# Kernel tuning notes

Measured on AMD Instinct MI355X. Metric: run time of the kernel, lower is better.

## Reference

```python
import jax, jax.numpy as jnp
import numpy as np

N_HEADS = 16


def setup_inputs() -> dict:
    key = jax.random.key(0)
    ks = jax.random.split(key, 5)
    B, S, D = 2, 2048, 1024
    H = N_HEADS
    return {
        "queries": jax.random.normal(ks[0], (B, S, D), dtype=jnp.float32),
        "keys": jax.random.normal(ks[1], (B, S, D), dtype=jnp.float32),
        "values": jax.random.normal(ks[2], (B, S, D), dtype=jnp.float32),
        "bias": jax.random.normal(ks[3], (1, H, S, S), dtype=jnp.float32) * 0.02,
        "w_out": jax.random.normal(ks[4], (D, D), dtype=jnp.float32) * (1.0 / np.sqrt(D)),
    }


def _split_heads(x, n_heads):
    B, S, D = x.shape
    return x.reshape(B, S, n_heads, D // n_heads).transpose(0, 2, 1, 3)  # [B,H,S,hd]


def reference(queries, keys, values, bias, w_out):
    H = N_HEADS
    q = _split_heads(queries, H)
    k = _split_heads(keys, H)
    v = _split_heads(values, H)
    hd = k.shape[-1]
    # NOTE: original adds bias to raw logits, THEN scales by 1/sqrt(dk)
    logits = jnp.einsum("bhqd,bhkd->bhqk", q, k) + bias
    weights = jax.nn.softmax(logits * (1.0 / np.sqrt(hd)), axis=-1)
    attn = jnp.einsum("bhqk,bhkd->bhqd", weights, v)  # [B,H,Sq,hd]
    B, _, Sq, _ = attn.shape
    combined = attn.transpose(0, 2, 1, 3).reshape(B, Sq, H * hd)
    return combined @ w_out
```

## Files before the change

### kernel.cpp

```cpp
#include <hip/hip_runtime.h>

typedef float  f32x4  __attribute__((ext_vector_type(4)));
typedef short  bf16x8 __attribute__((ext_vector_type(8)));
typedef short  s16x4  __attribute__((ext_vector_type(4)));
typedef unsigned int u32x4 __attribute__((ext_vector_type(4)));

#define MFMA_BF16 __builtin_amdgcn_mfma_f32_16x16x32_bf16

__device__ __forceinline__ short f2bf(float f) {
  __bf16 h = (__bf16)f;
  return __builtin_bit_cast(short, h);
}

constexpr int S = 2048, D = 1024, H = 16, HD = 64;
constexpr int NT = S / 64;
constexpr int NTH = NT / 2;
constexpr float SCALE = 0.125f;
constexpr float L2E = 1.44269504f;
constexpr float SL = SCALE * L2E;

#define GLDS16(g, l) __builtin_amdgcn_global_load_lds( \
    (const __attribute__((address_space(1))) unsigned*)(g), \
    (__attribute__((address_space(3))) unsigned*)(l), 16, 0, 0)

#define WAITV(n) asm volatile("s_waitcnt vmcnt(" #n ")" ::: "memory")
#define SBAR()   __builtin_amdgcn_s_barrier()

__global__ __launch_bounds__(256)
void kv_prep(const float* __restrict__ Kg, const float* __restrict__ Vg,
             short* __restrict__ KVb) {
  const int tile = blockIdx.x, h = blockIdx.y, b = blockIdx.z;
  const int t = threadIdx.x, lane = t & 63, w = t >> 6;
  const int lg = lane >> 4, lm = lane & 15;
  __shared__ short kt[64 * 68], vt[64 * 68];
  const float* kp = Kg + ((size_t)(b * S + tile * 64)) * D + h * HD;
  const float* vp = Vg + ((size_t)(b * S + tile * 64)) * D + h * HD;
  #pragma unroll
  for (int i = 0; i < 4; ++i) {
    int idx = i * 256 + t, r = idx >> 4, c4 = (idx & 15) * 4;
    float4 k4 = *(const float4*)(kp + (size_t)r * D + c4);
    s16x4 ks; ks[0]=f2bf(k4.x); ks[1]=f2bf(k4.y); ks[2]=f2bf(k4.z); ks[3]=f2bf(k4.w);
    *(s16x4*)&kt[r * 68 + c4] = ks;
    float4 v4 = *(const float4*)(vp + (size_t)r * D + c4);
    s16x4 vs; vs[0]=f2bf(v4.x); vs[1]=f2bf(v4.y); vs[2]=f2bf(v4.z); vs[3]=f2bf(v4.w);
    *(s16x4*)&vt[r * 68 + c4] = vs;
  }
  __syncthreads();
  const size_t obase = ((size_t)((b * H + h) * NT + tile)) * 8192;
  #pragma unroll
  for (int j = 0; j < 2; ++j) {
    int f = w + j * 4, kk = f >> 2, mf = f & 3;
    int row = mf * 16 + lm, col = kk * 32 + lg * 4;
    s16x4 c0 = *(const s16x4*)&kt[row * 68 + col];
    s16x4 c1 = *(const s16x4*)&kt[row * 68 + col + 16];
    bf16x8 a;
    a[0]=c0[0]; a[1]=c0[1]; a[2]=c0[2]; a[3]=c0[3];
    a[4]=c1[0]; a[5]=c1[1]; a[6]=c1[2]; a[7]=c1[3];
    *(bf16x8*)&KVb[obase + (size_t)(f * 64 + lane) * 8] = a;
  }
  #pragma unroll
  for (int j = 0; j < 2; ++j) {
    int fv = w + j * 4, kk = fv >> 2, of = fv & 3;
    int col = of * 16 + lm;
    bf16x8 a;
    #pragma unroll
    for (int half = 0; half < 2; ++half)
      #pragma unroll
      for (int e = 0; e < 4; ++e)
        a[half * 4 + e] = vt[(kk * 32 + lg * 4 + half * 16 + e) * 68 + col];
    *(bf16x8*)&KVb[obase + (size_t)((8 + fv) * 64 + lane) * 8] = a;
  }
}

__global__ __launch_bounds__(512, 4)
void attn_fused(const float* __restrict__ Qg, const float* __restrict__ Bg,
                const short* __restrict__ KVb,
                float* __restrict__ OP, float* __restrict__ ML) {
  __shared__ __attribute__((aligned(16))) short smem[16384];
  const int bid = blockIdx.x;
  const int c = bid & 7, g = bid >> 3;
  const int qb = g & 7, z = g >> 3;
  const int h = (c << 1) | (z & 1);
  const int b = (z >> 1) & 1;
  const int half = z >> 2;
  const int q0 = qb * 256;
  const int t = threadIdx.x, lane = t & 63, w = t >> 6;
  const int lg = lane >> 4, lm = lane & 15;

  bf16x8 qf[2][2];
  #pragma unroll
  for (int fq = 0; fq < 2; ++fq) {
    const float* qp = Qg + ((size_t)(b * S + q0 + w * 32 + fq * 16 + lm)) * D + h * HD;
    #pragma unroll
    for (int kk = 0; kk < 2; ++kk)
      #pragma unroll
      for (int j = 0; j < 8; ++j)
        qf[fq][kk][j] = f2bf(qp[kk * 32 + (j >> 2) * 16 + lg * 4 + (j & 3)]);
  }

  const short* KVt = KVb + ((size_t)((b * H + h) * NT + half * NTH)) * 8192;
  const float* bp = Bg + ((size_t)(h * S + q0 + w * 32 + lm)) * S + half * (NTH * 64) + lg * 4;

  const f32x4 zero4 = {0.f, 0.f, 0.f, 0.f};
  f32x4 o[2][4];
  #pragma unroll
  for (int fq = 0; fq < 2; ++fq)
    #pragma unroll
    for (int i = 0; i < 4; ++i) o[fq][i] = zero4;
  float M[2] = {-__builtin_inff(), -__builtin_inff()};
  float L[2] = {0.f, 0.f};
  f32x4 sacc[2][4];

#define STAGE(tile, buf)                                                \
  {                                                                     \
    const short* kvg_ = KVt + (size_t)(tile) * 8192;                    \
    _Pragma("unroll")                                                   \
    for (int f_ = 0; f_ < 2; ++f_) {                                    \
      int fr_ = w * 2 + f_;                                             \
      GLDS16(kvg_ + (size_t)(fr_ * 64 + lane) * 8, (buf) + fr_ * 512);  \
    }                                                                   \
  }

#define BLOAD(tile)                                                     \
  {                                                                     \
    _Pragma("unroll")                                                   \
    for (int fq_ = 0; fq_ < 2; ++fq_)                                   \
      _Pragma("unroll")                                                 \
      for (int mf_ = 0; mf_ < 4; ++mf_)                                 \
        sacc[fq_][mf_] = *(const f32x4*)(bp + (size_t)fq_ * 16 * S +    \
                                         (size_t)(tile) * 64 + mf_ * 16); \
  }

  STAGE(0, smem);
  BLOAD(0);

  for (int tt = 0; tt < NTH; ++tt) {
    SBAR();
    if (tt < NTH - 1) {
      STAGE(tt + 1, smem + ((tt + 1) & 1) * 8192);
      WAITV(10);
    } else {
      WAITV(8);
    }
    SBAR();
    const short* buf = smem + (tt & 1) * 8192;

    __builtin_amdgcn_s_setprio(1);
    #pragma unroll
    for (int kk = 0; kk < 2; ++kk)
      #pragma unroll
      for (int mf = 0; mf < 4; ++mf) {
        bf16x8 a = *(const bf16x8*)&buf[(kk * 4 + mf) * 512 + lane * 8];
        sacc[0][mf] = MFMA_BF16(a, qf[0][kk], sacc[0][mf], 0, 0, 0);
        sacc[1][mf] = MFMA_BF16(a, qf[1][kk], sacc[1][mf], 0, 0, 0);
      }
    __builtin_amdgcn_s_setprio(0);

    float tmax[2] = {-__builtin_inff(), -__builtin_inff()};
    #pragma unroll
    for (int fq = 0; fq < 2; ++fq)
      #pragma unroll
      for (int mf = 0; mf < 4; ++mf)
        #pragma unroll
        for (int j = 0; j < 4; ++j) {
          float tv = sacc[fq][mf][j] * SL;
          sacc[fq][mf][j] = tv;
          tmax[fq] = fmaxf(tmax[fq], tv);
        }
    #pragma unroll
    for (int fq = 0; fq < 2; ++fq) {
      tmax[fq] = fmaxf(tmax[fq], __shfl_xor(tmax[fq], 16, 64));
      tmax[fq] = fmaxf(tmax[fq], __shfl_xor(tmax[fq], 32, 64));
    }
    const int skip = (tmax[0] <= M[0]) && (tmax[1] <= M[1]);
    if (!__all(skip)) {
      #pragma unroll
      for (int fq = 0; fq < 2; ++fq) {
        float Mn = fmaxf(M[fq], tmax[fq]);
        float alpha = exp2f(M[fq] - Mn);
        #pragma unroll
        for (int of = 0; of < 4; ++of) {
          o[fq][of][0] *= alpha; o[fq][of][1] *= alpha;
          o[fq][of][2] *= alpha; o[fq][of][3] *= alpha;
        }
        L[fq] *= alpha;
        M[fq] = Mn;
      }
    }
    #pragma unroll
    for (int fq = 0; fq < 2; ++fq) {
      float psum = 0.f;
      #pragma unroll
      for (int mf = 0; mf < 4; ++mf)
        #pragma unroll
        for (int j = 0; j < 4; ++j) {
          float e = exp2f(sacc[fq][mf][j] - M[fq]);
          sacc[fq][mf][j] = e;
          psum += e;
        }
      psum += __shfl_xor(psum, 16, 64);
      psum += __shfl_xor(psum, 32, 64);
      L[fq] += psum;
    }
    bf16x8 pb[2][2];
    #pragma unroll
    for (int fq = 0; fq < 2; ++fq)
      #pragma unroll
      for (int kk = 0; kk < 2; ++kk)
        #pragma unroll
        for (int j = 0; j < 8; ++j)
          pb[fq][kk][j] = f2bf(sacc[fq][kk * 2 + (j >> 2)][j & 3]);

    if (tt < NTH - 1) BLOAD(tt + 1);

    __builtin_amdgcn_s_setprio(1);
    #pragma unroll
    for (int kk = 0; kk < 2; ++kk)
      #pragma unroll
      for (int of = 0; of < 4; ++of) {
        bf16x8 a = *(const bf16x8*)&buf[4096 + (kk * 4 + of) * 512 + lane * 8];
        o[0][of] = MFMA_BF16(a, pb[0][kk], o[0][of], 0, 0, 0);
        o[1][of] = MFMA_BF16(a, pb[1][kk], o[1][of], 0, 0, 0);
      }
    __builtin_amdgcn_s_setprio(0);
  }

  const int p = ((b * H + h) << 3) | qb;
  float* opb = OP + ((size_t)(half * 256 + p)) * 16384 + w * 2048;
  #pragma unroll
  for (int fq = 0; fq < 2; ++fq)
    #pragma unroll
    for (int of = 0; of < 4; ++of)
      *(f32x4*)&opb[(fq * 4 + of) * 256 + lane * 4] = o[fq][of];
  float* mlb = ML + ((size_t)(half * 256 + p)) * 512;
  if (lane < 16) {
    mlb[w * 32 + lm]        = M[0];
    mlb[w * 32 + 16 + lm]   = M[1];
    mlb[256 + w * 32 + lm]      = L[0];
    mlb[256 + w * 32 + 16 + lm] = L[1];
  }
#undef STAGE
#undef BLOAD
}

__global__ __launch_bounds__(256)
void combine(const float* __restrict__ OP, const float* __restrict__ ML,
             short* __restrict__ comb) {
  const int w = blockIdx.x & 7, p = blockIdx.x >> 3;
  const int b = p >> 7, h = (p >> 3) & 15, qb = p & 7;
  const int t = threadIdx.x, lane = t & 63, fr2 = t >> 6;
  __shared__ __attribute__((aligned(16))) short tile[32 * 72];
  const float* op0 = OP + (size_t)p * 16384 + w * 2048;
  const float* op1 = OP + (size_t)(256 + p) * 16384 + w * 2048;
  const float* ml0 = ML + (size_t)p * 512;
  const float* ml1 = ML + (size_t)(256 + p) * 512;
  #pragma unroll
  for (int ff = 0; ff < 2; ++ff) {
    int f = fr2 + ff * 4, fq = f >> 2, of = f & 3;
    int ql = fq * 16 + (lane & 15);
    int d  = of * 16 + (lane >> 4) * 4;
    float m0 = ml0[w * 32 + ql], m1 = ml1[w * 32 + ql];
    float l0 = ml0[256 + w * 32 + ql], l1 = ml1[256 + w * 32 + ql];
    float m = fmaxf(m0, m1);
    float a0 = exp2f(m0 - m), a1 = exp2f(m1 - m);
    float inv = 1.f / (l0 * a0 + l1 * a1);
    f32x4 v0 = *(const f32x4*)&op0[f * 256 + lane * 4];
    f32x4 v1 = *(const f32x4*)&op1[f * 256 + lane * 4];
    s16x4 r;
    #pragma unroll
    for (int j = 0; j < 4; ++j)
      r[j] = f2bf((v0[j] * a0 + v1[j] * a1) * inv);
    *(s16x4*)&tile[ql * 72 + d] = r;
  }
  __syncthreads();
  const int row = t >> 3, seg = t & 7;
  u32x4 u = *(const u32x4*)&tile[row * 72 + seg * 8];
  *(u32x4*)&comb[((size_t)(b * S + qb * 256 + w * 32 + row)) * D + h * HD + seg * 8] = u;
}

__global__ __launch_bounds__(256)
void wt_kernel(const float* __restrict__ W, short* __restrict__ Wt) {
  __shared__ __attribute__((aligned(16))) short tile[64 * 72];
  const int n0 = blockIdx.x * 64, k0 = blockIdx.y * 64;
  const int t = threadIdx.x;
  #pragma unroll
  for (int i = 0; i < 4; ++i) {
    int idx = i * 256 + t;
    int r  = idx >> 4, c4 = (idx & 15) * 4;
    float4 wv = *(const float4*)(W + (size_t)(k0 + r) * D + n0 + c4);
    tile[(c4 + 0) * 72 + r] = f2bf(wv.x);
    tile[(c4 + 1) * 72 + r] = f2bf(wv.y);
    tile[(c4 + 2) * 72 + r] = f2bf(wv.z);
    tile[(c4 + 3) * 72 + r] = f2bf(wv.w);
  }
  __syncthreads();
  #pragma unroll
  for (int it = 0; it < 2; ++it) {
    int idx = it * 256 + t;
    int r = idx >> 3, seg = idx & 7;
    u32x4 u = *(const u32x4*)&tile[r * 72 + seg * 8];
    *(u32x4*)&Wt[(size_t)(n0 + r) * D + k0 + seg * 8] = u;
  }
}

__device__ __forceinline__ bf16x8 ld_frag_swz(const short* base, int row, int kk, int lg) {
  const char* rp = (const char*)base + row * 128 + (lg & 1) * 8;
  int u0 = kk * 4 + (lg >> 1);
  int f  = row & 7;
  s16x4 c0 = *(const s16x4*)(rp + ((u0 ^ f) << 4));
  s16x4 c1 = *(const s16x4*)(rp + (((u0 + 2) ^ f) << 4));
  bf16x8 a;
  a[0]=c0[0]; a[1]=c0[1]; a[2]=c0[2]; a[3]=c0[3];
  a[4]=c1[0]; a[5]=c1[1]; a[6]=c1[2]; a[7]=c1[3];
  return a;
}

__global__ __launch_bounds__(256, 2)
void proj_gemm(const short* __restrict__ A, const short* __restrict__ Bt,
               float* __restrict__ C) {
  __shared__ __attribute__((aligned(16))) short a_lds[2][8192];
  __shared__ __attribute__((aligned(16))) short b_lds[2][4096];
  const int m0 = blockIdx.x * 128, n0 = blockIdx.y * 64;
  const int t = threadIdx.x, lane = t & 63, w = t >> 6;
  const int lg = lane >> 4, lm = lane & 15;
  const int srow = lane >> 3;
  const int sunit = (lane & 7) ^ srow;

  const f32x4 zero4 = {0.f, 0.f, 0.f, 0.f};
  f32x4 acc[2][4];
  #pragma unroll
  for (int i = 0; i < 2; ++i)
    #pragma unroll
    for (int j = 0; j < 4; ++j) acc[i][j] = zero4;

#define PSTAGE(ks, ab, bb)                                                  \
  {                                                                         \
    const short* ag_ = A  + (size_t)m0 * D + (ks) * 64;                     \
    const short* bg_ = Bt + (size_t)n0 * D + (ks) * 64;                     \
    _Pragma("unroll")                                                       \
    for (int i_ = 0; i_ < 4; ++i_) {                                        \
      int j_ = w * 4 + i_;                                                  \
      GLDS16(ag_ + (size_t)(j_ * 8 + srow) * D + sunit * 8, (ab) + j_ * 512); \
    }                                                                       \
    _Pragma("unroll")                                                       \
    for (int i_ = 0; i_ < 2; ++i_) {                                        \
      int j_ = w * 2 + i_;                                                  \
      GLDS16(bg_ + (size_t)(j_ * 8 + srow) * D + sunit * 8, (bb) + j_ * 512); \
    }                                                                       \
  }

#define PCOMPUTE(ab, bb)                                                    \
  {                                                                         \
    _Pragma("unroll")                                                       \
    for (int kk = 0; kk < 2; ++kk) {                                        \
      bf16x8 af0 = ld_frag_swz(ab, w * 32 + lm, kk, lg);                    \
      bf16x8 af1 = ld_frag_swz(ab, w * 32 + 16 + lm, kk, lg);               \
      bf16x8 bf0 = ld_frag_swz(bb, lm, kk, lg);                             \
      bf16x8 bf1 = ld_frag_swz(bb, 16 + lm, kk, lg);                        \
      bf16x8 bf2 = ld_frag_swz(bb, 32 + lm, kk, lg);                        \
      bf16x8 bf3 = ld_frag_swz(bb, 48 + lm, kk, lg);                        \
      __builtin_amdgcn_s_setprio(1);                                        \
      acc[0][0] = MFMA_BF16(af0, bf0, acc[0][0], 0, 0, 0);                  \
      acc[0][1] = MFMA_BF16(af0, bf1, acc[0][1], 0, 0, 0);                  \
      acc[0][2] = MFMA_BF16(af0, bf2, acc[0][2], 0, 0, 0);                  \
      acc[0][3] = MFMA_BF16(af0, bf3, acc[0][3], 0, 0, 0);                  \
      acc[1][0] = MFMA_BF16(af1, bf0, acc[1][0], 0, 0, 0);                  \
      acc[1][1] = MFMA_BF16(af1, bf1, acc[1][1], 0, 0, 0);                  \
      acc[1][2] = MFMA_BF16(af1, bf2, acc[1][2], 0, 0, 0);                  \
      acc[1][3] = MFMA_BF16(af1, bf3, acc[1][3], 0, 0, 0);                  \
      __builtin_amdgcn_s_setprio(0);                                        \
    }                                                                       \
  }

  PSTAGE(0, a_lds[0], b_lds[0]);
  for (int ks = 0; ks < 16; ks += 2) {
    SBAR();
    PSTAGE(ks + 1, a_lds[1], b_lds[1]);
    WAITV(6);
    SBAR();
    PCOMPUTE(a_lds[0], b_lds[0]);
    SBAR();
    if (ks + 2 < 16) {
      PSTAGE(ks + 2, a_lds[0], b_lds[0]);
      WAITV(6);
    } else {
      WAITV(0);
    }
    SBAR();
    PCOMPUTE(a_lds[1], b_lds[1]);
  }

  #pragma unroll
  for (int mf = 0; mf < 2; ++mf)
    #pragma unroll
    for (int j = 0; j < 4; ++j)
      #pragma unroll
      for (int nf = 0; nf < 4; ++nf)
        C[(size_t)(m0 + w * 32 + mf * 16 + lg * 4 + j) * D +
          n0 + nf * 16 + lm] = acc[mf][nf][j];
#undef PSTAGE
#undef PCOMPUTE
}

extern "C" void kernel_launch(void* const* d_in, const int* in_sizes, int n_in,
                              void* d_out, int out_size, void* d_ws, size_t ws_size,
                              hipStream_t stream) {
  const float* Qg = (const float*)d_in[0];
  const float* Kg = (const float*)d_in[1];
  const float* Vg = (const float*)d_in[2];
  const float* Bg = (const float*)d_in[3];
  const float* Wg = (const float*)d_in[4];
  float* out = (float*)d_out;

  short* comb = (short*)d_ws;
  short* Wt   = comb + (size_t)4096 * 1024;
  short* KVb  = Wt   + (size_t)1024 * 1024;
  float* OP   = (float*)(KVb + (size_t)2 * H * NT * 8192);
  float* ML   = OP + (size_t)2 * 256 * 16384;

  kv_prep<<<dim3(NT, H, 2), 256, 0, stream>>>(Kg, Vg, KVb);
  wt_kernel<<<dim3(D / 64, D / 64), 256, 0, stream>>>(Wg, Wt);
  attn_fused<<<dim3(512), 512, 0, stream>>>(Qg, Bg, KVb, OP, ML);
  combine<<<dim3(2048), 256, 0, stream>>>(OP, ML, comb);
  proj_gemm<<<dim3(32, 16), 256, 0, stream>>>(comb, Wt, out);
}
```

Before: 149.8 us.

## Prefetch bias into separate registers earlier, prime future bias rows, use fast exp2

Bias tiles now go into a separate register array, and the load for the next tile is issued right after the QK MFMAs instead of after the softmax, so more work covers it. Touch-loads two and three tiles ahead warm the cache for the bias stream. The pipeline now always issues a stage (clamped on the last iteration) so a single fixed vmcnt wait is used. exp2f and the division are replaced with the hardware exp2 and rcp intrinsics, trading a little accuracy for fewer instructions, while the extra bias registers add register pressure.

```diff
diff --git a/kernel.cpp b/kernel.cpp
--- a/kernel.cpp
+++ b/kernel.cpp
@@ -11,6 +11,7 @@
   __bf16 h = (__bf16)f;
   return __builtin_bit_cast(short, h);
 }
+__device__ __forceinline__ float fexp2(float x) { return __builtin_amdgcn_exp2f(x); }
 
 constexpr int S = 2048, D = 1024, H = 16, HD = 64;
 constexpr int NT = S / 64;
@@ -99,7 +100,8 @@
   }
 
   const short* KVt = KVb + ((size_t)((b * H + h) * NT + half * NTH)) * 8192;
-  const float* bp = Bg + ((size_t)(h * S + q0 + w * 32 + lm)) * S + half * (NTH * 64) + lg * 4;
+  const float* bp  = Bg + ((size_t)(h * S + q0 + w * 32 + lm)) * S + half * (NTH * 64) + lg * 4;
+  const float* bpr = Bg + ((size_t)(h * S + q0 + w * 32)) * S + half * (NTH * 64);
 
   const f32x4 zero4 = {0.f, 0.f, 0.f, 0.f};
   f32x4 o[2][4];
@@ -110,6 +112,7 @@
   float M[2] = {-__builtin_inff(), -__builtin_inff()};
   float L[2] = {0.f, 0.f};
   f32x4 sacc[2][4];
+  f32x4 biasN[2][4];
 
 #define STAGE(tile, buf)                                                \
   {                                                                     \
@@ -121,40 +124,56 @@
     }                                                                   \
   }
 
-#define BLOAD(tile)                                                     \
+#define BLOADN(tile)                                                    \
   {                                                                     \
     _Pragma("unroll")                                                   \
     for (int fq_ = 0; fq_ < 2; ++fq_)                                   \
       _Pragma("unroll")                                                 \
       for (int mf_ = 0; mf_ < 4; ++mf_)                                 \
-        sacc[fq_][mf_] = *(const f32x4*)(bp + (size_t)fq_ * 16 * S +    \
-                                         (size_t)(tile) * 64 + mf_ * 16); \
+        biasN[fq_][mf_] = *(const f32x4*)(bp + (size_t)fq_ * 16 * S +   \
+                                          (size_t)(tile) * 64 + mf_ * 16); \
+  }
+
+#define PRIME(tile)                                                     \
+  {                                                                     \
+    _Pragma("unroll")                                                   \
+    for (int i_ = 0; i_ < 2; ++i_) {                                    \
+      int il_ = i_ * 64 + lane;                                         \
+      float j_ = bpr[(size_t)(il_ >> 2) * S + (il_ & 3) * 16 + (size_t)(tile) * 64]; \
+      asm volatile("" :: "v"(j_));                                      \
+    }                                                                   \
   }
 
   STAGE(0, smem);
-  BLOAD(0);
+  BLOADN(0);
+  PRIME(1);
+  PRIME(2);
 
   for (int tt = 0; tt < NTH; ++tt) {
     SBAR();
-    if (tt < NTH - 1) {
-      STAGE(tt + 1, smem + ((tt + 1) & 1) * 8192);
-      WAITV(10);
-    } else {
-      WAITV(8);
-    }
+    { int st = (tt + 1 < NTH) ? tt + 1 : NTH - 1;
+      STAGE(st, smem + ((tt + 1) & 1) * 8192); }
+    WAITV(12);
     SBAR();
     const short* buf = smem + (tt & 1) * 8192;
 
     __builtin_amdgcn_s_setprio(1);
     #pragma unroll
-    for (int kk = 0; kk < 2; ++kk)
-      #pragma unroll
-      for (int mf = 0; mf < 4; ++mf) {
-        bf16x8 a = *(const bf16x8*)&buf[(kk * 4 + mf) * 512 + lane * 8];
-        sacc[0][mf] = MFMA_BF16(a, qf[0][kk], sacc[0][mf], 0, 0, 0);
-        sacc[1][mf] = MFMA_BF16(a, qf[1][kk], sacc[1][mf], 0, 0, 0);
-      }
+    for (int mf = 0; mf < 4; ++mf) {
+      bf16x8 a = *(const bf16x8*)&buf[mf * 512 + lane * 8];
+      sacc[0][mf] = MFMA_BF16(a, qf[0][0], biasN[0][mf], 0, 0, 0);
+      sacc[1][mf] = MFMA_BF16(a, qf[1][0], biasN[1][mf], 0, 0, 0);
+    }
+    #pragma unroll
+    for (int mf = 0; mf < 4; ++mf) {
+      bf16x8 a = *(const bf16x8*)&buf[(4 + mf) * 512 + lane * 8];
+      sacc[0][mf] = MFMA_BF16(a, qf[0][1], sacc[0][mf], 0, 0, 0);
+      sacc[1][mf] = MFMA_BF16(a, qf[1][1], sacc[1][mf], 0, 0, 0);
+    }
     __builtin_amdgcn_s_setprio(0);
+
+    { int nt_ = (tt + 1 < NTH) ? tt + 1 : NTH - 1; BLOADN(nt_); }
+    { int pt_ = (tt + 3 < NTH) ? tt + 3 : NTH - 1; PRIME(pt_); }
 
     float tmax[2] = {-__builtin_inff(), -__builtin_inff()};
     #pragma unroll
@@ -177,7 +196,7 @@
       #pragma unroll
       for (int fq = 0; fq < 2; ++fq) {
         float Mn = fmaxf(M[fq], tmax[fq]);
-        float alpha = exp2f(M[fq] - Mn);
+        float alpha = fexp2(M[fq] - Mn);
         #pragma unroll
         for (int of = 0; of < 4; ++of) {
           o[fq][of][0] *= alpha; o[fq][of][1] *= alpha;
@@ -194,7 +213,7 @@
       for (int mf = 0; mf < 4; ++mf)
         #pragma unroll
         for (int j = 0; j < 4; ++j) {
-          float e = exp2f(sacc[fq][mf][j] - M[fq]);
+          float e = fexp2(sacc[fq][mf][j] - M[fq]);
           sacc[fq][mf][j] = e;
           psum += e;
         }
@@ -210,8 +229,6 @@
         #pragma unroll
         for (int j = 0; j < 8; ++j)
           pb[fq][kk][j] = f2bf(sacc[fq][kk * 2 + (j >> 2)][j & 3]);
-
-    if (tt < NTH - 1) BLOAD(tt + 1);
 
     __builtin_amdgcn_s_setprio(1);
     #pragma unroll
@@ -240,7 +257,8 @@
     mlb[256 + w * 32 + 16 + lm] = L[1];
   }
 #undef STAGE
-#undef BLOAD
+#undef BLOADN
+#undef PRIME
 }
 
 __global__ __launch_bounds__(256)
@@ -262,8 +280,8 @@
     float m0 = ml0[w * 32 + ql], m1 = ml1[w * 32 + ql];
     float l0 = ml0[256 + w * 32 + ql], l1 = ml1[256 + w * 32 + ql];
     float m = fmaxf(m0, m1);
-    float a0 = exp2f(m0 - m), a1 = exp2f(m1 - m);
-    float inv = 1.f / (l0 * a0 + l1 * a1);
+    float a0 = fexp2(m0 - m), a1 = fexp2(m1 - m);
+    float inv = __builtin_amdgcn_rcpf(l0 * a0 + l1 * a1);
     f32x4 v0 = *(const f32x4*)&op0[f * 256 + lane * 4];
     f32x4 v1 = *(const f32x4*)&op1[f * 256 + lane * 4];
     s16x4 r;
```

After: 293.1 us. +95.6%, slower.
